# Kernel optimization log

Hardware: AMD Instinct MI355X
Metric: run time of the kernel (lower is better)

## Reference

```python
import jax, jax.numpy as jnp
import numpy as np

B, S, DIM, E, K = 8, 8192, 512, 4, 2
EPS = 1e-6


def setup_inputs() -> dict:
    key = jax.random.key(0)
    ks = jax.random.split(key, 4)
    scale = 0.02
    return {
        "x": jax.random.normal(ks[0], (B, S, DIM), dtype=jnp.float32),
        "router_w": jax.random.normal(ks[1], (DIM, E), dtype=jnp.float32) * scale,
        "router_b": jnp.zeros((E,), jnp.float32),
        "expert_w": jax.random.normal(ks[2], (E, DIM, DIM), dtype=jnp.float32) * scale,
        "expert_b": jnp.zeros((E, DIM), jnp.float32),
        "out_w": jax.random.normal(ks[3], (DIM, DIM), dtype=jnp.float32) * scale,
        "out_b": jnp.zeros((DIM,), jnp.float32),
        "norm_w": jnp.ones((DIM,), jnp.float32),
    }


def reference(x, router_w, router_b, expert_w, expert_b, out_w, out_b, norm_w):
    b, s, d = x.shape
    # router
    logits = x @ router_w + router_b                      # [B,S,E]
    topw, topi = jax.lax.top_k(logits, K)                 # [B,S,K]
    topw = jax.nn.softmax(topw, axis=-1)
    t = b * s
    xf = x.reshape(t, d)
    idx = topi.reshape(t, K)
    w = topw.reshape(t, K).astype(x.dtype)
    # dense token-expert weight mask (topk indices are distinct per token)
    mask = jnp.zeros((t, E), x.dtype).at[jnp.arange(t)[:, None], idx].set(w)
    # expert FFN: Linear + SiLU (dropout disabled in eval)
    h = jax.nn.silu(jnp.einsum("td,edh->teh", xf, expert_w) + expert_b)  # [T,E,D]
    comb = jnp.einsum("te,teh->th", mask, h)              # weighted combine
    out = comb @ out_w + out_b
    y = xf + out                                          # residual
    rms = jnp.sqrt(jnp.mean(y * y, axis=-1, keepdims=True) + EPS)
    return (norm_w * (y / rms)).reshape(b, s, d)
```

## Files before the change

kernel.cpp:

```cpp
#include <hip/hip_runtime.h>
#include <hip/hip_bf16.h>
#include <stdint.h>

#define NTOK 65536
#define DIM 512
#define NEXP 4
#define REG 14336

using u16 = unsigned short;
using u32 = unsigned int;
typedef __attribute__((ext_vector_type(4))) float f32x4;
typedef __attribute__((ext_vector_type(8))) short bf16x8;
typedef __attribute__((ext_vector_type(8))) u16 u16x8;

__device__ __forceinline__ u16 f2bf(float f) {
  u32 u = __builtin_bit_cast(u32, f);
  u32 r = (u + 0x7FFFu + ((u >> 16) & 1u)) >> 16;
  return (u16)r;
}

#define GLOAD_LDS16(gp, lp)                                                    \
  __builtin_amdgcn_global_load_lds(                                            \
      (const __attribute__((address_space(1))) void*)(gp),                     \
      (__attribute__((address_space(3))) void*)(lp), 16, 0, 0)

#define FENCE asm volatile("" ::: "memory")
#define BARRIER { FENCE; __builtin_amdgcn_s_barrier(); FENCE; }
#define LGKM0 { asm volatile("s_waitcnt lgkmcnt(0)" ::: "memory"); __builtin_amdgcn_sched_barrier(0); }
#define VMCNT_(n) asm volatile("s_waitcnt vmcnt(" #n ")" ::: "memory")
#define VMCNT(n) VMCNT_(n)

__device__ __forceinline__ const bf16x8* lds_frag(const u16* base, int row, int chunk) {
  return (const bf16x8*)((const char*)base + row * 128 + (((chunk) ^ (row & 7)) << 4));
}
__device__ __forceinline__ const bf16x8* frag32(const u16* base, int row, int rchByte) {
  return (const bf16x8*)((const char*)base + row * 64 + rchByte);
}

__global__ void wconv(const float* __restrict__ ew, const float* __restrict__ ow,
                      u16* __restrict__ ewt, u16* __restrict__ owt, int* __restrict__ cnt) {
  __shared__ float tile[32][33];
  int mat = blockIdx.y;
  if (blockIdx.x == 0 && mat == 0 && threadIdx.x < 6) cnt[threadIdx.x] = 0;
  const float* s = (mat < 4) ? ew + (size_t)mat * DIM * DIM : ow;
  u16* d = (mat < 4) ? ewt + (size_t)mat * DIM * DIM : owt;
  int tx = blockIdx.x & 15, ty = blockIdx.x >> 4;
  int lx = threadIdx.x & 31, ly0 = threadIdx.x >> 5;
#pragma unroll
  for (int i = 0; i < 4; ++i) {
    int ly = ly0 + i * 8;
    tile[ly][lx] = s[(size_t)(ty * 32 + ly) * DIM + tx * 32 + lx];
  }
  __syncthreads();
#pragma unroll
  for (int i = 0; i < 4; ++i) {
    int ly = ly0 + i * 8;
    d[(size_t)(tx * 32 + ly) * DIM + ty * 32 + lx] = f2bf(tile[lx][ly]);
  }
}

__global__ void router_kernel(const float* __restrict__ x, const float* __restrict__ rw,
                              const float* __restrict__ rb, u16* __restrict__ xb,
                              int* __restrict__ pp, float2* __restrict__ wab) {
  int lane = threadIdx.x & 63, wave = threadIdx.x >> 6;
  size_t t = (size_t)blockIdx.x * 4 + wave;
  const float* xr = x + t * DIM + lane * 8;
  f32x4 v0 = *(const f32x4*)xr;
  f32x4 v1 = *(const f32x4*)(xr + 4);
  float l0 = 0.f, l1 = 0.f, l2 = 0.f, l3 = 0.f;
  const float* rwp = rw + (size_t)lane * 32;
#pragma unroll
  for (int j = 0; j < 8; ++j) {
    float xv = (j < 4) ? v0[j] : v1[j - 4];
    f32x4 r = *(const f32x4*)(rwp + j * 4);
    l0 += xv * r[0]; l1 += xv * r[1]; l2 += xv * r[2]; l3 += xv * r[3];
  }
#pragma unroll
  for (int off = 32; off; off >>= 1) {
    l0 += __shfl_xor(l0, off); l1 += __shfl_xor(l1, off);
    l2 += __shfl_xor(l2, off); l3 += __shfl_xor(l3, off);
  }
  float lv[4] = {l0 + rb[0], l1 + rb[1], l2 + rb[2], l3 + rb[3]};
  int i0 = 0; float b0 = lv[0];
#pragma unroll
  for (int e = 1; e < 4; ++e) if (lv[e] > b0) { b0 = lv[e]; i0 = e; }
  int i1 = (i0 == 0) ? 1 : 0; float b1 = lv[i1];
#pragma unroll
  for (int e = 0; e < 4; ++e) if (e != i0 && lv[e] > b1) { b1 = lv[e]; i1 = e; }
  float ex = __expf(b1 - b0);
  float w0 = 1.0f / (1.0f + ex);
  float w1 = ex * w0;
  if (lane == 0) {
    int a = (i0 < i1) ? i0 : i1;
    int b = (i0 < i1) ? i1 : i0;
    const int ptab[16] = {-1, 0, 1, 2, -1, -1, 3, 4, -1, -1, -1, 5, -1, -1, -1, -1};
    pp[t] = ptab[a * 4 + b];
    float wa = (a == i0) ? w0 : w1;
    float wb = (a == i0) ? w1 : w0;
    wab[t] = make_float2(wa, wb);
  }
  u16x8 o;
#pragma unroll
  for (int j = 0; j < 4; ++j) { o[j] = f2bf(v0[j]); o[4 + j] = f2bf(v1[j]); }
  *(u16x8*)(xb + t * DIM + lane * 8) = o;
}

__global__ void assignscatter(const int* __restrict__ pp, const float2* __restrict__ wab,
                              int* __restrict__ cnt, int* __restrict__ list,
                              float2* __restrict__ wpair) {
  int t = blockIdx.x * 256 + threadIdx.x;
  int lane = threadIdx.x & 63;
  int p = pp[t];
  float2 w = wab[t];
  int pos = 0;
#pragma unroll
  for (int q = 0; q < 6; ++q) {
    unsigned long long m = __ballot(p == q);
    if (p == q) {
      int rank = __popcll(m & ((1ull << lane) - 1ull));
      int leader = __ffsll((long long)m) - 1;
      int base = 0;
      if (lane == leader) base = atomicAdd(&cnt[q], (int)__popcll(m));
      base = __shfl(base, leader);
      pos = base + rank;
    }
  }
  int slot = p * REG + pos;
  if (pos < REG) {
    list[slot] = t;
    wpair[slot] = w;
  }
}

__global__ __launch_bounds__(256, 2) void expert_gemm(
    const u16* __restrict__ xb, const u16* __restrict__ ewt,
    const float* __restrict__ ebias, const int* __restrict__ cnt,
    const int* __restrict__ list, const float2* __restrict__ wpair,
    u16* __restrict__ comb) {
  __shared__ u16 Asl[3][128 * 32];
  __shared__ u16 Bal[3][128 * 32];
  __shared__ u16 Bbl[3][128 * 32];
  int tid = threadIdx.x, lane = tid & 63, wave = tid >> 6;
  int wy = wave >> 1, wx = wave & 1;
  int b = blockIdx.x;
  int chunk = b >> 5, within = b & 31;
  int panel = chunk * 8 + (within & 7);
  int nblk = within >> 3;
  int p = panel / (REG / 128);
  int m0 = panel * 128;
  int cntp = cnt[p];
  if (m0 - p * REG >= cntp) return;
  int n0 = nblk * 128;
  const int ea2[6] = {0, 0, 0, 1, 1, 2};
  const int eb2[6] = {1, 2, 3, 2, 3, 3};
  int eA = ea2[p], eB = eb2[p];

  int r4 = lane >> 2, c4 = lane & 3;
  int rot = (r4 >> 1) & 3;
  int kch = ((c4 - rot) & 3) * 8;
  int r16 = lane & 15, lg = lane >> 4;
  int rchB = (((lg + ((r16 >> 1) & 3)) & 3)) * 16;

  int sid2[2];
#pragma unroll
  for (int j = 0; j < 2; ++j) {
    int slot = m0 + wave * 32 + j * 16 + r4;
    int idv = list[slot];
    sid2[j] = ((slot - p * REG) < cntp) ? idv : 0;
  }

  f32x4 accA[4][4], accB[4][4];
#pragma unroll
  for (int i = 0; i < 4; ++i)
#pragma unroll
    for (int j = 0; j < 4; ++j) { accA[i][j] = (f32x4)(0.f); accB[i][j] = (f32x4)(0.f); }

#define STAGE(bi, ks)                                                          \
  do {                                                                         \
    _Pragma("unroll") for (int j = 0; j < 2; ++j) {                            \
      GLOAD_LDS16(xb + (size_t)sid2[j] * DIM + (ks) * 32 + kch,                \
                  Asl[bi] + (wave * 32 + j * 16) * 32);                        \
    }                                                                          \
    _Pragma("unroll") for (int j = 0; j < 2; ++j) {                            \
      int hr = n0 + wave * 32 + j * 16 + r4;                                   \
      GLOAD_LDS16(ewt + (size_t)eA * DIM * DIM + (size_t)hr * DIM + (ks) * 32 + kch, \
                  Bal[bi] + (wave * 32 + j * 16) * 32);                        \
      GLOAD_LDS16(ewt + (size_t)eB * DIM * DIM + (size_t)hr * DIM + (ks) * 32 + kch, \
                  Bbl[bi] + (wave * 32 + j * 16) * 32);                        \
    }                                                                          \
  } while (0)

  STAGE(0, 0); STAGE(1, 1); STAGE(2, 2);
  VMCNT(12);
  BARRIER;

  int cur = 0;
#pragma unroll 1
  for (int t = 0; t < 16; ++t) {
    const u16* As_ = Asl[cur];
    const u16* Ba_ = Bal[cur];
    const u16* Bb_ = Bbl[cur];
    bf16x8 a[4], ba[4], bb[4];
#pragma unroll
    for (int i = 0; i < 4; ++i) {
      a[i]  = *frag32(As_, wy * 64 + i * 16 + r16, rchB);
      ba[i] = *frag32(Ba_, wx * 64 + i * 16 + r16, rchB);
      bb[i] = *frag32(Bb_, wx * 64 + i * 16 + r16, rchB);
    }
    __builtin_amdgcn_s_setprio(1);
#pragma unroll
    for (int i = 0; i < 4; ++i)
#pragma unroll
      for (int j = 0; j < 4; ++j)
        accA[i][j] = __builtin_amdgcn_mfma_f32_16x16x32_bf16(a[i], ba[j], accA[i][j], 0, 0, 0);
    __builtin_amdgcn_s_setprio(0);
    LGKM0;
    BARRIER;
    if (t + 3 < 16) STAGE(cur, t + 3);
    __builtin_amdgcn_s_setprio(1);
#pragma unroll
    for (int i = 0; i < 4; ++i)
#pragma unroll
      for (int j = 0; j < 4; ++j)
        accB[i][j] = __builtin_amdgcn_mfma_f32_16x16x32_bf16(a[i], bb[j], accB[i][j], 0, 0, 0);
    __builtin_amdgcn_s_setprio(0);
    if (t < 13) { VMCNT(12); BARRIER; }
    else if (t == 13) { VMCNT(6); BARRIER; }
    else if (t == 14) { VMCNT(0); BARRIER; }
    cur = (cur == 2) ? 0 : cur + 1;
  }
#undef STAGE

  float bA4[4], bB4[4];
#pragma unroll
  for (int j = 0; j < 4; ++j) {
    int h = n0 + wx * 64 + j * 16 + r16;
    bA4[j] = ebias[eA * DIM + h];
    bB4[j] = ebias[eB * DIM + h];
  }
#pragma unroll
  for (int i = 0; i < 4; ++i) {
    int rb = wy * 64 + i * 16 + lg * 4;
#pragma unroll
    for (int rr = 0; rr < 4; ++rr) {
      int slot = m0 + rb + rr;
      bool val = (slot - p * REG) < cntp;
      int id = list[slot];
      float2 wv = wpair[slot];
#pragma unroll
      for (int j = 0; j < 4; ++j) {
        float zA = accA[i][j][rr] + bA4[j];
        float zB = accB[i][j][rr] + bB4[j];
        float sA = zA / (1.0f + __expf(-zA));
        float sB = zB / (1.0f + __expf(-zB));
        float v = wv.x * sA + wv.y * sB;
        if (val) {
          int h = n0 + wx * 64 + j * 16 + r16;
          comb[(size_t)id * DIM + h] = f2bf(v);
        }
      }
    }
  }
}

__global__ __launch_bounds__(256, 2) void outnorm(
    const u16* __restrict__ comb, const u16* __restrict__ owt,
    const float* __restrict__ ob, const float* __restrict__ x,
    const float* __restrict__ nw, float* __restrict__ out) {
  __shared__ u16 As[2][64 * 64];
  __shared__ float rowsum[64][4];
  int tid = threadIdx.x, lane = tid & 63, w = tid >> 6;
  int m0 = blockIdx.x * 64;
  int r16 = lane & 15, lg = lane >> 4;
  int rl = lane >> 3;
  int scb = ((lane & 7) ^ rl) * 8;
  int n0w = w * 128;

  f32x4 acc[4][8];
#pragma unroll
  for (int i = 0; i < 4; ++i)
#pragma unroll
    for (int j = 0; j < 8; ++j) acc[i][j] = (f32x4)(0.f);

#define OSTG(bi, ks)                                                           \
  _Pragma("unroll") for (int j = 0; j < 2; ++j) {                              \
    GLOAD_LDS16(comb + (size_t)(m0 + w * 16 + j * 8 + rl) * DIM + (ks) * 64 + scb, \
                As[bi] + (w * 16 + j * 8) * 64);                               \
  }

  OSTG(0, 0);
  __syncthreads();
#pragma unroll 1
  for (int t = 0; t < 8; ++t) {
    if (t + 1 < 8) OSTG((t + 1) & 1, t + 1);
    const u16* Ab = As[t & 1];
    bf16x8 af[8];
#pragma unroll
    for (int i = 0; i < 4; ++i) {
      af[i * 2]     = *lds_frag(Ab, i * 16 + r16, lg);
      af[i * 2 + 1] = *lds_frag(Ab, i * 16 + r16, 4 + lg);
    }
#pragma unroll
    for (int kc = 0; kc < 2; ++kc) {
      bf16x8 bfr[8];
#pragma unroll
      for (int j = 0; j < 8; ++j)
        bfr[j] = *(const bf16x8*)(owt + (size_t)(n0w + j * 16 + r16) * DIM +
                                  t * 64 + kc * 32 + lg * 8);
      __builtin_amdgcn_s_setprio(1);
#pragma unroll
      for (int i = 0; i < 4; ++i)
#pragma unroll
        for (int j = 0; j < 8; ++j)
          acc[i][j] = __builtin_amdgcn_mfma_f32_16x16x32_bf16(af[i * 2 + kc], bfr[j], acc[i][j], 0, 0, 0);
      __builtin_amdgcn_s_setprio(0);
    }
    __syncthreads();
  }
#undef OSTG

  float part[4][4];
#pragma unroll
  for (int i = 0; i < 4; ++i)
#pragma unroll
    for (int rr = 0; rr < 4; ++rr) part[i][rr] = 0.f;
#pragma unroll
  for (int i = 0; i < 4; ++i) {
#pragma unroll
    for (int j = 0; j < 8; ++j) {
      int h = n0w + j * 16 + r16;
      float bias = ob[h];
#pragma unroll
      for (int rr = 0; rr < 4; ++rr) {
        int lr = i * 16 + lg * 4 + rr;
        float yv = x[(size_t)(m0 + lr) * DIM + h] + acc[i][j][rr] + bias;
        acc[i][j][rr] = yv;
        part[i][rr] += yv * yv;
      }
    }
  }
#pragma unroll
  for (int off = 1; off < 16; off <<= 1)
#pragma unroll
    for (int i = 0; i < 4; ++i)
#pragma unroll
      for (int rr = 0; rr < 4; ++rr) part[i][rr] += __shfl_xor(part[i][rr], off);
  if (r16 == 0) {
#pragma unroll
    for (int i = 0; i < 4; ++i)
#pragma unroll
      for (int rr = 0; rr < 4; ++rr)
        rowsum[i * 16 + lg * 4 + rr][w] = part[i][rr];
  }
  __syncthreads();
  float inv[4][4];
#pragma unroll
  for (int i = 0; i < 4; ++i)
#pragma unroll
    for (int rr = 0; rr < 4; ++rr) {
      int lr = i * 16 + lg * 4 + rr;
      float s = rowsum[lr][0] + rowsum[lr][1] + rowsum[lr][2] + rowsum[lr][3];
      inv[i][rr] = 1.0f / sqrtf(s * (1.0f / 512.0f) + 1e-6f);
    }
#pragma unroll
  for (int i = 0; i < 4; ++i) {
#pragma unroll
    for (int j = 0; j < 8; ++j) {
      int h = n0w + j * 16 + r16;
      float wv = nw[h];
#pragma unroll
      for (int rr = 0; rr < 4; ++rr) {
        int lr = i * 16 + lg * 4 + rr;
        out[(size_t)(m0 + lr) * DIM + h] = acc[i][j][rr] * inv[i][rr] * wv;
      }
    }
  }
}

extern "C" void kernel_launch(void* const* d_in, const int* in_sizes, int n_in,
                              void* d_out, int out_size, void* d_ws, size_t ws_size,
                              hipStream_t stream) {
  const float* x  = (const float*)d_in[0];
  const float* rw = (const float*)d_in[1];
  const float* rb = (const float*)d_in[2];
  const float* ew = (const float*)d_in[3];
  const float* eb = (const float*)d_in[4];
  const float* ow = (const float*)d_in[5];
  const float* ob = (const float*)d_in[6];
  const float* nw = (const float*)d_in[7];
  float* out = (float*)d_out;

  char* ws = (char*)d_ws;
  u16*   xb    = (u16*)(ws);
  u16*   combb = (u16*)(ws + 67108864);
  int*   pp    = (int*)(ws + 67108864);
  float2* wab  = (float2*)(ws + 67108864 + 262144);
  u16*   ewt   = (u16*)(ws + 134217728);
  u16*   owt   = (u16*)(ws + 136314880);
  int*   list  = (int*)(ws + 136839168);
  float2* wpair = (float2*)(ws + 136839168 + 344064);
  int*   cnt   = (int*)(ws + 136839168 + 344064 + 688128);

  wconv<<<dim3(256, 5), 256, 0, stream>>>(ew, ow, ewt, owt, cnt);
  router_kernel<<<NTOK / 4, 256, 0, stream>>>(x, rw, rb, xb, pp, wab);
  assignscatter<<<NTOK / 256, 256, 0, stream>>>(pp, wab, cnt, list, wpair);
  expert_gemm<<<dim3(6 * REG / 128 * 4), 256, 0, stream>>>(xb, ewt, eb, cnt, list, wpair, combb);
  outnorm<<<dim3(NTOK / 64), 256, 0, stream>>>(combb, owt, ob, x, nw, out);
}
```

Baseline: 369.7 us.

## Use 256-row tiles with 8 waves and a 4-stage fully unrolled pipeline in expert GEMM

The expert GEMM block grows from 256 to 512 threads and from 128 to 256 token rows per tile, so each block of B (expert weight) data is reused across twice as many rows. The LDS ring goes from 3 to 4 stages, which lets the mid-iteration lgkmcnt wait and barrier be dropped and the next stage be issued at the top of each k-step. The k-loop is fully unrolled with constant buffer indices. In exchange, occupancy drops to one block per CU, LDS use grows, and panels covering partly filled expert regions waste more rows.

```diff
diff --git a/kernel.cpp b/kernel.cpp
--- a/kernel.cpp
+++ b/kernel.cpp
@@ -26,7 +26,6 @@
 
 #define FENCE asm volatile("" ::: "memory")
 #define BARRIER { FENCE; __builtin_amdgcn_s_barrier(); FENCE; }
-#define LGKM0 { asm volatile("s_waitcnt lgkmcnt(0)" ::: "memory"); __builtin_amdgcn_sched_barrier(0); }
 #define VMCNT_(n) asm volatile("s_waitcnt vmcnt(" #n ")" ::: "memory")
 #define VMCNT(n) VMCNT_(n)
 
@@ -132,22 +131,22 @@
   }
 }
 
-__global__ __launch_bounds__(256, 2) void expert_gemm(
+__global__ __launch_bounds__(512, 1) void expert_gemm(
     const u16* __restrict__ xb, const u16* __restrict__ ewt,
     const float* __restrict__ ebias, const int* __restrict__ cnt,
     const int* __restrict__ list, const float2* __restrict__ wpair,
     u16* __restrict__ comb) {
-  __shared__ u16 Asl[3][128 * 32];
-  __shared__ u16 Bal[3][128 * 32];
-  __shared__ u16 Bbl[3][128 * 32];
+  __shared__ u16 Asl[4][256 * 32];
+  __shared__ u16 Bal[4][128 * 32];
+  __shared__ u16 Bbl[4][128 * 32];
   int tid = threadIdx.x, lane = tid & 63, wave = tid >> 6;
   int wy = wave >> 1, wx = wave & 1;
   int b = blockIdx.x;
   int chunk = b >> 5, within = b & 31;
   int panel = chunk * 8 + (within & 7);
   int nblk = within >> 3;
-  int p = panel / (REG / 128);
-  int m0 = panel * 128;
+  int p = panel / (REG / 256);
+  int m0 = panel * 256;
   int cntp = cnt[p];
   if (m0 - p * REG >= cntp) return;
   int n0 = nblk * 128;
@@ -159,15 +158,17 @@
   int rot = (r4 >> 1) & 3;
   int kch = ((c4 - rot) & 3) * 8;
   int r16 = lane & 15, lg = lane >> 4;
-  int rchB = (((lg + ((r16 >> 1) & 3)) & 3)) * 16;
-
-  int sid2[2];
-#pragma unroll
-  for (int j = 0; j < 2; ++j) {
-    int slot = m0 + wave * 32 + j * 16 + r4;
-    int idv = list[slot];
-    sid2[j] = ((slot - p * REG) < cntp) ? idv : 0;
-  }
+  int rchB = ((lg + ((r16 >> 1) & 3)) & 3) * 16;
+
+  int slotA0 = m0 + wave * 32 + r4;
+  int slotA1 = slotA0 + 16;
+  int idv0 = list[slotA0], idv1 = list[slotA1];
+  int sid0 = ((slotA0 - p * REG) < cntp) ? idv0 : 0;
+  int sid1 = ((slotA1 - p * REG) < cntp) ? idv1 : 0;
+  const u16* abase0 = xb + (size_t)sid0 * DIM + kch;
+  const u16* abase1 = xb + (size_t)sid1 * DIM + kch;
+  const u16* babase = ewt + (size_t)eA * DIM * DIM + (size_t)(n0 + wave * 16 + r4) * DIM + kch;
+  const u16* bbbase = ewt + (size_t)eB * DIM * DIM + (size_t)(n0 + wave * 16 + r4) * DIM + kch;
 
   f32x4 accA[4][4], accB[4][4];
 #pragma unroll
@@ -175,61 +176,60 @@
 #pragma unroll
     for (int j = 0; j < 4; ++j) { accA[i][j] = (f32x4)(0.f); accB[i][j] = (f32x4)(0.f); }
 
-#define STAGE(bi, ks)                                                          \
+#define STG(T)                                                                 \
   do {                                                                         \
-    _Pragma("unroll") for (int j = 0; j < 2; ++j) {                            \
-      GLOAD_LDS16(xb + (size_t)sid2[j] * DIM + (ks) * 32 + kch,                \
-                  Asl[bi] + (wave * 32 + j * 16) * 32);                        \
+    const int SB_ = (T) & 3;                                                   \
+    GLOAD_LDS16(abase0 + (T) * 32, Asl[SB_] + (wave * 32) * 32);               \
+    GLOAD_LDS16(abase1 + (T) * 32, Asl[SB_] + (wave * 32 + 16) * 32);          \
+    GLOAD_LDS16(babase + (T) * 32, Bal[SB_] + (wave * 16) * 32);               \
+    GLOAD_LDS16(bbbase + (T) * 32, Bbl[SB_] + (wave * 16) * 32);               \
+  } while (0)
+
+  STG(0); STG(1); STG(2);
+  VMCNT(8);
+  BARRIER;
+
+#define KSTEP(T, SEN, WCODE)                                                   \
+  {                                                                            \
+    const int BUF_ = (T) & 3;                                                  \
+    if (SEN) STG((T) + 3);                                                     \
+    bf16x8 a_[4], ba_[4], bb_[4];                                              \
+    _Pragma("unroll") for (int i = 0; i < 4; ++i) {                            \
+      a_[i]  = *frag32(Asl[BUF_], wy * 64 + i * 16 + r16, rchB);               \
+      ba_[i] = *frag32(Bal[BUF_], wx * 64 + i * 16 + r16, rchB);               \
+      bb_[i] = *frag32(Bbl[BUF_], wx * 64 + i * 16 + r16, rchB);               \
     }                                                                          \
-    _Pragma("unroll") for (int j = 0; j < 2; ++j) {                            \
-      int hr = n0 + wave * 32 + j * 16 + r4;                                   \
-      GLOAD_LDS16(ewt + (size_t)eA * DIM * DIM + (size_t)hr * DIM + (ks) * 32 + kch, \
-                  Bal[bi] + (wave * 32 + j * 16) * 32);                        \
-      GLOAD_LDS16(ewt + (size_t)eB * DIM * DIM + (size_t)hr * DIM + (ks) * 32 + kch, \
-                  Bbl[bi] + (wave * 32 + j * 16) * 32);                        \
-    }                                                                          \
-  } while (0)
-
-  STAGE(0, 0); STAGE(1, 1); STAGE(2, 2);
-  VMCNT(12);
-  BARRIER;
-
-  int cur = 0;
-#pragma unroll 1
-  for (int t = 0; t < 16; ++t) {
-    const u16* As_ = Asl[cur];
-    const u16* Ba_ = Bal[cur];
-    const u16* Bb_ = Bbl[cur];
-    bf16x8 a[4], ba[4], bb[4];
-#pragma unroll
-    for (int i = 0; i < 4; ++i) {
-      a[i]  = *frag32(As_, wy * 64 + i * 16 + r16, rchB);
-      ba[i] = *frag32(Ba_, wx * 64 + i * 16 + r16, rchB);
-      bb[i] = *frag32(Bb_, wx * 64 + i * 16 + r16, rchB);
-    }
-    __builtin_amdgcn_s_setprio(1);
-#pragma unroll
-    for (int i = 0; i < 4; ++i)
-#pragma unroll
-      for (int j = 0; j < 4; ++j)
-        accA[i][j] = __builtin_amdgcn_mfma_f32_16x16x32_bf16(a[i], ba[j], accA[i][j], 0, 0, 0);
-    __builtin_amdgcn_s_setprio(0);
-    LGKM0;
-    BARRIER;
-    if (t + 3 < 16) STAGE(cur, t + 3);
-    __builtin_amdgcn_s_setprio(1);
-#pragma unroll
-    for (int i = 0; i < 4; ++i)
-#pragma unroll
-      for (int j = 0; j < 4; ++j)
-        accB[i][j] = __builtin_amdgcn_mfma_f32_16x16x32_bf16(a[i], bb[j], accB[i][j], 0, 0, 0);
-    __builtin_amdgcn_s_setprio(0);
-    if (t < 13) { VMCNT(12); BARRIER; }
-    else if (t == 13) { VMCNT(6); BARRIER; }
-    else if (t == 14) { VMCNT(0); BARRIER; }
-    cur = (cur == 2) ? 0 : cur + 1;
-  }
-#undef STAGE
+    __builtin_amdgcn_s_setprio(1);                                             \
+    _Pragma("unroll") for (int i = 0; i < 4; ++i)                              \
+      _Pragma("unroll") for (int j = 0; j < 4; ++j)                            \
+        accA[i][j] = __builtin_amdgcn_mfma_f32_16x16x32_bf16(a_[i], ba_[j], accA[i][j], 0, 0, 0); \
+    __builtin_amdgcn_s_setprio(0);                                             \
+    __builtin_amdgcn_s_setprio(1);                                             \
+    _Pragma("unroll") for (int i = 0; i < 4; ++i)                              \
+      _Pragma("unroll") for (int j = 0; j < 4; ++j)                            \
+        accB[i][j] = __builtin_amdgcn_mfma_f32_16x16x32_bf16(a_[i], bb_[j], accB[i][j], 0, 0, 0); \
+    __builtin_amdgcn_s_setprio(0);                                             \
+    WCODE;                                                                     \
+  }
+
+  KSTEP(0, 1, { VMCNT(8); BARRIER; })
+  KSTEP(1, 1, { VMCNT(8); BARRIER; })
+  KSTEP(2, 1, { VMCNT(8); BARRIER; })
+  KSTEP(3, 1, { VMCNT(8); BARRIER; })
+  KSTEP(4, 1, { VMCNT(8); BARRIER; })
+  KSTEP(5, 1, { VMCNT(8); BARRIER; })
+  KSTEP(6, 1, { VMCNT(8); BARRIER; })
+  KSTEP(7, 1, { VMCNT(8); BARRIER; })
+  KSTEP(8, 1, { VMCNT(8); BARRIER; })
+  KSTEP(9, 1, { VMCNT(8); BARRIER; })
+  KSTEP(10, 1, { VMCNT(8); BARRIER; })
+  KSTEP(11, 1, { VMCNT(8); BARRIER; })
+  KSTEP(12, 1, { VMCNT(8); BARRIER; })
+  KSTEP(13, 0, { VMCNT(4); BARRIER; })
+  KSTEP(14, 0, { VMCNT(0); BARRIER; })
+  KSTEP(15, 0, {})
+#undef KSTEP
+#undef STG
 
   float bA4[4], bB4[4];
 #pragma unroll
@@ -404,6 +404,6 @@
   wconv<<<dim3(256, 5), 256, 0, stream>>>(ew, ow, ewt, owt, cnt);
   router_kernel<<<NTOK / 4, 256, 0, stream>>>(x, rw, rb, xb, pp, wab);
   assignscatter<<<NTOK / 256, 256, 0, stream>>>(pp, wab, cnt, list, wpair);
-  expert_gemm<<<dim3(6 * REG / 128 * 4), 256, 0, stream>>>(xb, ewt, eb, cnt, list, wpair, combb);
+  expert_gemm<<<dim3(6 * REG / 256 * 4), 512, 0, stream>>>(xb, ewt, eb, cnt, list, wpair, combb);
   outnorm<<<dim3(NTOK / 64), 256, 0, stream>>>(combb, owt, ob, x, nw, out);
 }
```

Result: slower. 378.6 us (+2.4%).

## Pre-pack out_w into MFMA fragment order and triple-buffer outnorm pipeline

Applied to the files above, without the earlier changes.

Adds an owpack kernel that stores the output projection weights as bf16 in the exact per-lane MFMA B-fragment order, so outnorm can load each fragment with one contiguous 16-byte load per lane instead of strided row reads. The outnorm main loop is unrolled into 16 half-steps with a 3-stage LDS ring for the comb tile and double-buffered B-fragment registers, using explicit vmcnt waits and barriers. The aim is to overlap global loads with MFMA work and cut load latency stalls. In exchange it uses more LDS and registers, which may lower occupancy, and relies on hand-tuned wait counts.

```diff
diff --git a/kernel.cpp b/kernel.cpp
--- a/kernel.cpp
+++ b/kernel.cpp
@@ -37,13 +37,13 @@
   return (const bf16x8*)((const char*)base + row * 64 + rchByte);
 }
 
-__global__ void wconv(const float* __restrict__ ew, const float* __restrict__ ow,
-                      u16* __restrict__ ewt, u16* __restrict__ owt, int* __restrict__ cnt) {
+__global__ void wconv(const float* __restrict__ ew, u16* __restrict__ ewt,
+                      int* __restrict__ cnt) {
   __shared__ float tile[32][33];
   int mat = blockIdx.y;
   if (blockIdx.x == 0 && mat == 0 && threadIdx.x < 6) cnt[threadIdx.x] = 0;
-  const float* s = (mat < 4) ? ew + (size_t)mat * DIM * DIM : ow;
-  u16* d = (mat < 4) ? ewt + (size_t)mat * DIM * DIM : owt;
+  const float* s = ew + (size_t)mat * DIM * DIM;
+  u16* d = ewt + (size_t)mat * DIM * DIM;
   int tx = blockIdx.x & 15, ty = blockIdx.x >> 4;
   int lx = threadIdx.x & 31, ly0 = threadIdx.x >> 5;
 #pragma unroll
@@ -57,6 +57,19 @@
     int ly = ly0 + i * 8;
     d[(size_t)(tx * 32 + ly) * DIM + ty * 32 + lx] = f2bf(tile[lx][ly]);
   }
+}
+
+__global__ void owpack(const float* __restrict__ ow, u16* __restrict__ owt3) {
+  int lane = threadIdx.x & 63, wv = threadIdx.x >> 6;
+  int frag = blockIdx.x * 4 + wv;
+  int j = frag & 7, kc = (frag >> 3) & 1, t = (frag >> 4) & 7, strip = frag >> 7;
+  int r16 = lane & 15, lg = lane >> 4;
+  int h = strip * 128 + j * 16 + r16;
+  int d0 = t * 64 + kc * 32 + lg * 8;
+  u16x8 o;
+#pragma unroll
+  for (int q = 0; q < 8; ++q) o[q] = f2bf(ow[(size_t)(d0 + q) * DIM + h]);
+  *(u16x8*)(owt3 + (size_t)frag * 512 + lane * 8) = o;
 }
 
 __global__ void router_kernel(const float* __restrict__ x, const float* __restrict__ rw,
@@ -264,10 +277,10 @@
 }
 
 __global__ __launch_bounds__(256, 2) void outnorm(
-    const u16* __restrict__ comb, const u16* __restrict__ owt,
+    const u16* __restrict__ comb, const u16* __restrict__ owt3,
     const float* __restrict__ ob, const float* __restrict__ x,
     const float* __restrict__ nw, float* __restrict__ out) {
-  __shared__ u16 As[2][64 * 64];
+  __shared__ u16 As[3][64 * 64];
   __shared__ float rowsum[64][4];
   int tid = threadIdx.x, lane = tid & 63, w = tid >> 6;
   int m0 = blockIdx.x * 64;
@@ -283,40 +296,57 @@
     for (int j = 0; j < 8; ++j) acc[i][j] = (f32x4)(0.f);
 
 #define OSTG(bi, ks)                                                           \
-  _Pragma("unroll") for (int j = 0; j < 2; ++j) {                              \
-    GLOAD_LDS16(comb + (size_t)(m0 + w * 16 + j * 8 + rl) * DIM + (ks) * 64 + scb, \
-                As[bi] + (w * 16 + j * 8) * 64);                               \
-  }
-
-  OSTG(0, 0);
-  __syncthreads();
-#pragma unroll 1
-  for (int t = 0; t < 8; ++t) {
-    if (t + 1 < 8) OSTG((t + 1) & 1, t + 1);
-    const u16* Ab = As[t & 1];
-    bf16x8 af[8];
-#pragma unroll
-    for (int i = 0; i < 4; ++i) {
-      af[i * 2]     = *lds_frag(Ab, i * 16 + r16, lg);
-      af[i * 2 + 1] = *lds_frag(Ab, i * 16 + r16, 4 + lg);
-    }
-#pragma unroll
-    for (int kc = 0; kc < 2; ++kc) {
-      bf16x8 bfr[8];
-#pragma unroll
-      for (int j = 0; j < 8; ++j)
-        bfr[j] = *(const bf16x8*)(owt + (size_t)(n0w + j * 16 + r16) * DIM +
-                                  t * 64 + kc * 32 + lg * 8);
-      __builtin_amdgcn_s_setprio(1);
-#pragma unroll
-      for (int i = 0; i < 4; ++i)
-#pragma unroll
-        for (int j = 0; j < 8; ++j)
-          acc[i][j] = __builtin_amdgcn_mfma_f32_16x16x32_bf16(af[i * 2 + kc], bfr[j], acc[i][j], 0, 0, 0);
-      __builtin_amdgcn_s_setprio(0);
-    }
-    __syncthreads();
-  }
+  _Pragma("unroll") for (int jj = 0; jj < 2; ++jj) {                           \
+    GLOAD_LDS16(comb + (size_t)(m0 + w * 16 + jj * 8 + rl) * DIM + (ks) * 64 + scb, \
+                As[bi] + (w * 16 + jj * 8) * 64);                              \
+  }
+#define LOADB(BV, HH)                                                          \
+  {                                                                            \
+    const u16* bp_ = owt3 +                                                    \
+        ((size_t)(((w * 8 + ((HH) >> 1)) * 2 + ((HH) & 1)) * 8)) * 512 + lane * 8; \
+    _Pragma("unroll") for (int jj = 0; jj < 8; ++jj)                           \
+      BV[jj] = *(const bf16x8*)(bp_ + jj * 512);                               \
+  }
+#define HSTEP(H, BC, BN, WC)                                                   \
+  {                                                                            \
+    if (((H) & 1) == 0 && ((H) >> 1) + 2 < 8) OSTG((((H) >> 1) + 2) % 3, ((H) >> 1) + 2); \
+    if ((H) + 1 < 16) LOADB(BN, (H) + 1);                                      \
+    bf16x8 af[4];                                                              \
+    _Pragma("unroll") for (int ii = 0; ii < 4; ++ii)                           \
+      af[ii] = *lds_frag(As[((H) >> 1) % 3], ii * 16 + r16, ((H) & 1) * 4 + lg); \
+    LGKM0;                                                                     \
+    __builtin_amdgcn_s_setprio(1);                                             \
+    _Pragma("unroll") for (int ii = 0; ii < 4; ++ii)                           \
+      _Pragma("unroll") for (int jj = 0; jj < 8; ++jj)                         \
+        acc[ii][jj] = __builtin_amdgcn_mfma_f32_16x16x32_bf16(af[ii], BC[jj], acc[ii][jj], 0, 0, 0); \
+    __builtin_amdgcn_s_setprio(0);                                             \
+    WC;                                                                        \
+  }
+
+  bf16x8 BE[8], BO[8];
+  OSTG(0, 0); OSTG(1, 1);
+  LOADB(BE, 0);
+  VMCNT(10);
+  BARRIER;
+
+  HSTEP(0,  BE, BO, {})
+  HSTEP(1,  BO, BE, { VMCNT(10); BARRIER; })
+  HSTEP(2,  BE, BO, {})
+  HSTEP(3,  BO, BE, { VMCNT(10); BARRIER; })
+  HSTEP(4,  BE, BO, {})
+  HSTEP(5,  BO, BE, { VMCNT(10); BARRIER; })
+  HSTEP(6,  BE, BO, {})
+  HSTEP(7,  BO, BE, { VMCNT(10); BARRIER; })
+  HSTEP(8,  BE, BO, {})
+  HSTEP(9,  BO, BE, { VMCNT(10); BARRIER; })
+  HSTEP(10, BE, BO, {})
+  HSTEP(11, BO, BE, { VMCNT(10); BARRIER; })
+  HSTEP(12, BE, BO, {})
+  HSTEP(13, BO, BE, { VMCNT(8); BARRIER; })
+  HSTEP(14, BE, BO, {})
+  HSTEP(15, BO, BE, {})
+#undef HSTEP
+#undef LOADB
 #undef OSTG
 
   float part[4][4];
@@ -396,14 +426,15 @@
   int*   pp    = (int*)(ws + 67108864);
   float2* wab  = (float2*)(ws + 67108864 + 262144);
   u16*   ewt   = (u16*)(ws + 134217728);
-  u16*   owt   = (u16*)(ws + 136314880);
+  u16*   owt3  = (u16*)(ws + 136314880);
   int*   list  = (int*)(ws + 136839168);
   float2* wpair = (float2*)(ws + 136839168 + 344064);
   int*   cnt   = (int*)(ws + 136839168 + 344064 + 688128);
 
-  wconv<<<dim3(256, 5), 256, 0, stream>>>(ew, ow, ewt, owt, cnt);
+  wconv<<<dim3(256, 4), 256, 0, stream>>>(ew, ewt, cnt);
+  owpack<<<128, 256, 0, stream>>>(ow, owt3);
   router_kernel<<<NTOK / 4, 256, 0, stream>>>(x, rw, rb, xb, pp, wab);
   assignscatter<<<NTOK / 256, 256, 0, stream>>>(pp, wab, cnt, list, wpair);
   expert_gemm<<<dim3(6 * REG / 128 * 4), 256, 0, stream>>>(xb, ewt, eb, cnt, list, wpair, combb);
-  outnorm<<<dim3(NTOK / 64), 256, 0, stream>>>(combb, owt, ob, x, nw, out);
-}
+  outnorm<<<dim3(NTOK / 64), 256, 0, stream>>>(combb, owt3, ob, x, nw, out);
+}
```

After: 347.6 us. 6.0% less time.
